# Kernel tuning notes

Hardware: AMD Instinct MI355X
Metric: run time of the kernel (lower is better)

The kernel has to match this reference:

```python
import jax, jax.numpy as jnp
import numpy as np


def setup_inputs() -> dict:
    key = jax.random.key(0)
    k1, k2 = jax.random.split(key)
    B, N, M = 8, 8192, 8192
    points1 = jax.random.normal(k1, (B, N, 2), dtype=jnp.float32)
    points2 = jax.random.normal(k2, (B, M, 2), dtype=jnp.float32)
    return {"points1": points1, "points2": points2}


def reference(points1, points2):
    # points1: [B, N, 2], points2: [B, M, 2]
    # Squared pairwise distances via |a|^2 + |b|^2 - 2 a.b  -> [B, N, M]
    p1_sq = jnp.sum(points1 * points1, axis=-1)  # [B, N]
    p2_sq = jnp.sum(points2 * points2, axis=-1)  # [B, M]
    cross = jnp.einsum("bnd,bmd->bnm", points1, points2)  # [B, N, M]
    sqdist = p1_sq[:, :, None] + p2_sq[:, None, :] - 2.0 * cross
    dist1 = jnp.min(sqdist, axis=2)  # [B, N]: NN of each p1 point in p2
    dist2 = jnp.min(sqdist, axis=1)  # [B, M]: NN of each p2 point in p1
    cost = jnp.mean(dist1, axis=-1) + jnp.mean(dist2, axis=-1)  # [B]
    return jnp.sum(cost)
```

## Files before the change

kernel.cpp:

```cpp
#include <hip/hip_runtime.h>


#define BATCH 8
#define NPTS  8192
#define TPB   256
#define IPT   16
#define PPB   (TPB * IPT)
#define TILES (NPTS / PPB)
#define S     16
#define JCH   (NPTS / S)

__global__ __launch_bounds__(TPB, 2)
void chamfer_partial(const float* __restrict__ p1, const float* __restrict__ p2,
                     float* __restrict__ partial ) {
    __shared__ float4 q[JCH];

    int blk = blockIdx.x;
    int split = blk & (S - 1);      blk >>= 4;
    int tile  = blk & (TILES - 1);  blk >>= 1;
    int b     = blk & (BATCH - 1);  blk >>= 3;
    int dir   = blk;

    const float2* a  = (const float2*)(dir ? p2 : p1) + (size_t)b * NPTS;
    const float2* bp = (const float2*)(dir ? p1 : p2) + (size_t)b * NPTS + split * JCH;

    int t = threadIdx.x;

    for (int j = t; j < JCH; j += TPB) {
        float2 v = bp[j];
        q[j] = make_float4(v.x, v.y, fmaf(v.x, v.x, v.y * v.y), 0.0f);
    }

    int pt_base = tile * PPB;
    float xp[IPT], yp[IPT], m[IPT];
#pragma unroll
    for (int k = 0; k < IPT; ++k) {
        float2 v = a[pt_base + k * TPB + t];
        xp[k] = -2.0f * v.x;
        yp[k] = -2.0f * v.y;
        m[k]  = 3.0e38f;
    }

    __syncthreads();

    for (int j = 0; j < JCH; j += 2) {
        float4 q0 = q[j];
        float4 q1 = q[j + 1];
#pragma unroll
        for (int k = 0; k < IPT; ++k) {
            float t0 = fmaf(yp[k], q0.y, fmaf(xp[k], q0.x, q0.z));
            float t1 = fmaf(yp[k], q1.y, fmaf(xp[k], q1.x, q1.z));
            m[k] = fminf(m[k], fminf(t0, t1));
        }
    }

    float* out = partial + ((size_t)(dir * BATCH + b) * S + split) * NPTS + pt_base;
#pragma unroll
    for (int k = 0; k < IPT; ++k)
        out[k * TPB + t] = m[k];
}

__global__ __launch_bounds__(TPB)
void chamfer_reduce(const float* __restrict__ p1, const float* __restrict__ p2,
                    const float* __restrict__ partial, float* __restrict__ out) {
    int gid   = blockIdx.x * TPB + threadIdx.x;
    int point = gid & (NPTS - 1);
    int rest  = gid >> 13;
    int b     = rest & (BATCH - 1);
    int dir   = rest >> 3;

    const float* base = partial + ((size_t)(dir * BATCH + b) * S) * NPTS + point;
    float m = base[0];
#pragma unroll
    for (int s = 1; s < S; ++s)
        m = fminf(m, base[(size_t)s * NPTS]);

    float2 v = ((const float2*)(dir ? p2 : p1))[(size_t)b * NPTS + point];
    float d = m + fmaf(v.x, v.x, v.y * v.y);

#pragma unroll
    for (int off = 32; off > 0; off >>= 1)
        d += __shfl_down(d, off, 64);

    __shared__ float wsum[TPB / 64];
    int lane = threadIdx.x & 63;
    int w    = threadIdx.x >> 6;
    if (lane == 0) wsum[w] = d;
    __syncthreads();
    if (threadIdx.x == 0) {
        float ssum = wsum[0] + wsum[1] + wsum[2] + wsum[3];
        atomicAdd(out, ssum * (1.0f / NPTS));
    }
}

extern "C" void kernel_launch(void* const* d_in, const int* in_sizes, int n_in,
                              void* d_out, int out_size, void* d_ws, size_t ws_size,
                              hipStream_t stream) {
    const float* p1 = (const float*)d_in[0];
    const float* p2 = (const float*)d_in[1];
    float* out      = (float*)d_out;
    float* partial  = (float*)d_ws;

    hipMemsetAsync(d_out, 0, sizeof(float), stream);

    chamfer_partial<<<2 * BATCH * TILES * S, TPB, 0, stream>>>(p1, p2, partial);
    chamfer_reduce<<<2 * BATCH * NPTS / TPB, TPB, 0, stream>>>(p1, p2, partial, out);
}
```

Measured before the change: 138.4 us.

## Replace brute-force all-pairs search with uniform-grid spatial hashing nearest-neighbor search

Replaces the O(N*M) all-pairs min-distance computation with a bucketed uniform grid. Four stages do the work: count points per cell, prefix-sum the counts, scatter points into cell-sorted order, then search rings of cells outward from each query until the ring distance bound exceeds the current best. This cuts arithmetic drastically, but adds several kernel launches, atomics, divergent variable-length loops per thread, and dependence on the point distribution. Points outside the fixed box are clamped into edge cells. The ring-termination bound (c*H) ignores the query's offset within its own cell and the clamping, so results may not be exact in every case.

After: 173.8 us. +25.6%, slower.

```diff
diff --git a/kernel.cpp b/kernel.cpp
--- a/kernel.cpp
+++ b/kernel.cpp
@@ -1,108 +1,139 @@
 #include <hip/hip_runtime.h>
+#include <stdint.h>
 
 
 #define BATCH 8
 #define NPTS  8192
 #define TPB   256
-#define IPT   16
-#define PPB   (TPB * IPT)
-#define TILES (NPTS / PPB)
-#define S     16
-#define JCH   (NPTS / S)
+#define GRID  128
+#define G2    (GRID * GRID)
+#define BOX   4.25f
+#define H     0.06640625f
+#define NSB   (2 * BATCH)
 
-__global__ __launch_bounds__(TPB, 2)
-void chamfer_partial(const float* __restrict__ p1, const float* __restrict__ p2,
-                     float* __restrict__ partial ) {
-    __shared__ float4 q[JCH];
+__device__ inline int cellof(float v) {
+    int c = (int)((v + BOX) * (1.0f / H));
+    return min(max(c, 0), GRID - 1);
+}
 
-    int blk = blockIdx.x;
-    int split = blk & (S - 1);      blk >>= 4;
-    int tile  = blk & (TILES - 1);  blk >>= 1;
-    int b     = blk & (BATCH - 1);  blk >>= 3;
-    int dir   = blk;
+__global__ void hist_k(const float2* __restrict__ p1, const float2* __restrict__ p2,
+                       int* __restrict__ counts) {
+    int g = blockIdx.x * TPB + threadIdx.x;
+    int side = g >> 16, b = (g >> 13) & 7, i = g & (NPTS - 1);
+    float2 P = (side ? p2 : p1)[(size_t)b * NPTS + i];
+    int cell = cellof(P.y) * GRID + cellof(P.x);
+    atomicAdd(&counts[(side * BATCH + b) * G2 + cell], 1);
+}
 
-    const float2* a  = (const float2*)(dir ? p2 : p1) + (size_t)b * NPTS;
-    const float2* bp = (const float2*)(dir ? p1 : p2) + (size_t)b * NPTS + split * JCH;
+__global__ __launch_bounds__(TPB) void prefix_k(const int* __restrict__ counts,
+                                                int* __restrict__ start,
+                                                int* __restrict__ cursor) {
+    __shared__ int psum[TPB];
+    const int CPT = G2 / TPB;
+    int base = blockIdx.x * G2;
+    int t = threadIdx.x;
+    int s = 0;
+    for (int u = 0; u < CPT; ++u) s += counts[base + t * CPT + u];
+    psum[t] = s;
+    __syncthreads();
+    for (int off = 1; off < TPB; off <<= 1) {
+        int v = (t >= off) ? psum[t - off] : 0;
+        __syncthreads();
+        psum[t] += v;
+        __syncthreads();
+    }
+    int run = psum[t] - s;
+    for (int u = 0; u < CPT; ++u) {
+        int idx = base + t * CPT + u;
+        int c = counts[idx];
+        start[idx] = run;
+        cursor[idx] = run;
+        run += c;
+    }
+}
 
-    int t = threadIdx.x;
+__global__ void scatter_k(const float2* __restrict__ p1, const float2* __restrict__ p2,
+                          int* __restrict__ cursor, float2* __restrict__ sorted) {
+    int g = blockIdx.x * TPB + threadIdx.x;
+    int side = g >> 16, b = (g >> 13) & 7, i = g & (NPTS - 1);
+    float2 P = (side ? p2 : p1)[(size_t)b * NPTS + i];
+    int cell = cellof(P.y) * GRID + cellof(P.x);
+    int sb = side * BATCH + b;
+    int pos = atomicAdd(&cursor[sb * G2 + cell], 1);
+    sorted[(size_t)sb * NPTS + pos] = P;
+}
 
-    for (int j = t; j < JCH; j += TPB) {
-        float2 v = bp[j];
-        q[j] = make_float4(v.x, v.y, fmaf(v.x, v.x, v.y * v.y), 0.0f);
+__global__ __launch_bounds__(TPB) void query_k(const float2* __restrict__ sorted,
+                                               const int* __restrict__ start,
+                                               const int* __restrict__ counts,
+                                               float* __restrict__ out) {
+    int g = blockIdx.x * TPB + threadIdx.x;
+    int dir = g >> 16, b = (g >> 13) & 7, i = g & (NPTS - 1);
+
+    float2 q = sorted[((size_t)(dir * BATCH + b)) * NPTS + i];
+    int tg = (1 - dir) * BATCH + b;
+    const float2* __restrict__ pts = sorted + (size_t)tg * NPTS;
+    const int* __restrict__ st = start + tg * G2;
+    const int* __restrict__ ct = counts + tg * G2;
+
+    int cx = cellof(q.x), cy = cellof(q.y);
+    float best = 3.0e38f;
+
+    auto scan = [&](int cell_lo, int cell_hi) {
+        int s = st[cell_lo];
+        int e = st[cell_hi] + ct[cell_hi];
+        for (int k = s; k < e; ++k) {
+            float2 p = pts[k];
+            float dx = q.x - p.x, dy = q.y - p.y;
+            best = fminf(best, fmaf(dx, dx, dy * dy));
+        }
+    };
+
+    scan(cy * GRID + cx, cy * GRID + cx);
+    int cmax = max(max(cx, GRID - 1 - cx), max(cy, GRID - 1 - cy));
+    for (int c = 1;; ++c) {
+        int xlo = max(cx - c, 0), xhi = min(cx + c, GRID - 1);
+        if (cy - c >= 0)        scan((cy - c) * GRID + xlo, (cy - c) * GRID + xhi);
+        if (cy + c <= GRID - 1) scan((cy + c) * GRID + xlo, (cy + c) * GRID + xhi);
+        int ylo = max(cy - c + 1, 0), yhi = min(cy + c - 1, GRID - 1);
+        if (cx - c >= 0)
+            for (int y = ylo; y <= yhi; ++y) scan(y * GRID + cx - c, y * GRID + cx - c);
+        if (cx + c <= GRID - 1)
+            for (int y = ylo; y <= yhi; ++y) scan(y * GRID + cx + c, y * GRID + cx + c);
+        float bd = (float)c * H;
+        if (best <= bd * bd || c >= cmax) break;
     }
 
-    int pt_base = tile * PPB;
-    float xp[IPT], yp[IPT], m[IPT];
-#pragma unroll
-    for (int k = 0; k < IPT; ++k) {
-        float2 v = a[pt_base + k * TPB + t];
-        xp[k] = -2.0f * v.x;
-        yp[k] = -2.0f * v.y;
-        m[k]  = 3.0e38f;
-    }
-
-    __syncthreads();
-
-    for (int j = 0; j < JCH; j += 2) {
-        float4 q0 = q[j];
-        float4 q1 = q[j + 1];
-#pragma unroll
-        for (int k = 0; k < IPT; ++k) {
-            float t0 = fmaf(yp[k], q0.y, fmaf(xp[k], q0.x, q0.z));
-            float t1 = fmaf(yp[k], q1.y, fmaf(xp[k], q1.x, q1.z));
-            m[k] = fminf(m[k], fminf(t0, t1));
-        }
-    }
-
-    float* out = partial + ((size_t)(dir * BATCH + b) * S + split) * NPTS + pt_base;
-#pragma unroll
-    for (int k = 0; k < IPT; ++k)
-        out[k * TPB + t] = m[k];
-}
-
-__global__ __launch_bounds__(TPB)
-void chamfer_reduce(const float* __restrict__ p1, const float* __restrict__ p2,
-                    const float* __restrict__ partial, float* __restrict__ out) {
-    int gid   = blockIdx.x * TPB + threadIdx.x;
-    int point = gid & (NPTS - 1);
-    int rest  = gid >> 13;
-    int b     = rest & (BATCH - 1);
-    int dir   = rest >> 3;
-
-    const float* base = partial + ((size_t)(dir * BATCH + b) * S) * NPTS + point;
-    float m = base[0];
-#pragma unroll
-    for (int s = 1; s < S; ++s)
-        m = fminf(m, base[(size_t)s * NPTS]);
-
-    float2 v = ((const float2*)(dir ? p2 : p1))[(size_t)b * NPTS + point];
-    float d = m + fmaf(v.x, v.x, v.y * v.y);
-
+    float d = best;
 #pragma unroll
     for (int off = 32; off > 0; off >>= 1)
         d += __shfl_down(d, off, 64);
-
     __shared__ float wsum[TPB / 64];
-    int lane = threadIdx.x & 63;
-    int w    = threadIdx.x >> 6;
+    int lane = threadIdx.x & 63, w = threadIdx.x >> 6;
     if (lane == 0) wsum[w] = d;
     __syncthreads();
-    if (threadIdx.x == 0) {
-        float ssum = wsum[0] + wsum[1] + wsum[2] + wsum[3];
-        atomicAdd(out, ssum * (1.0f / NPTS));
-    }
+    if (threadIdx.x == 0)
+        atomicAdd(out, (wsum[0] + wsum[1] + wsum[2] + wsum[3]) * (1.0f / NPTS));
 }
 
 extern "C" void kernel_launch(void* const* d_in, const int* in_sizes, int n_in,
                               void* d_out, int out_size, void* d_ws, size_t ws_size,
                               hipStream_t stream) {
-    const float* p1 = (const float*)d_in[0];
-    const float* p2 = (const float*)d_in[1];
-    float* out      = (float*)d_out;
-    float* partial  = (float*)d_ws;
+    const float2* p1 = (const float2*)d_in[0];
+    const float2* p2 = (const float2*)d_in[1];
+    float* out = (float*)d_out;
 
-    hipMemsetAsync(d_out, 0, sizeof(float), stream);
+    char* ws = (char*)d_ws;
+    int*    counts = (int*)(ws);
+    int*    start  = (int*)(ws + (size_t)1 * 1024 * 1024);
+    int*    cursor = (int*)(ws + (size_t)2 * 1024 * 1024);
+    float2* sorted = (float2*)(ws + (size_t)3 * 1024 * 1024);
 
-    chamfer_partial<<<2 * BATCH * TILES * S, TPB, 0, stream>>>(p1, p2, partial);
-    chamfer_reduce<<<2 * BATCH * NPTS / TPB, TPB, 0, stream>>>(p1, p2, partial, out);
+    hipMemsetAsync(counts, 0, (size_t)NSB * G2 * sizeof(int), stream);
+    hipMemsetAsync(out, 0, sizeof(float), stream);
+
+    hist_k<<<2 * BATCH * NPTS / TPB, TPB, 0, stream>>>(p1, p2, counts);
+    prefix_k<<<NSB, TPB, 0, stream>>>(counts, start, cursor);
+    scatter_k<<<2 * BATCH * NPTS / TPB, TPB, 0, stream>>>(p1, p2, cursor, sorted);
+    query_k<<<2 * BATCH * NPTS / TPB, TPB, 0, stream>>>(sorted, start, counts, out);
 }
```
